# Kernel tuning notes

Hardware: AMD Instinct MI355X
Metric: run time of the kernel (lower is better)

## Reference

```python
import jax, jax.numpy as jnp
import numpy as np

M, TS, NX, NY = 24, 60, 192, 192   # solutions, source timesteps, source grid
H, D = 4, 8                         # num_heads, d_head
SIGMA = 0.2
N_TIME_STEPS = 50
T_MAX = 200.0
LX = 100.0                          # solutions[0]['params']['Lx']
SRC_T_MAX = 200.0                   # solutions[0]['params']['t_max']
NG = 50                             # target grid resolution (hard-coded in source)


def setup_inputs():
    key = jax.random.key(0)
    ks = jax.random.split(key, 8)
    c1_preds = jax.random.normal(ks[0], (M, TS, NX, NY), jnp.float32)
    c2_preds = jax.random.normal(ks[1], (M, TS, NX, NY), jnp.float32)
    lys = 30.0 + 90.0 * jax.random.uniform(ks[2], (M,), jnp.float32)
    c_cus = 0.0029 * jax.random.uniform(ks[3], (M,), jnp.float32)
    c_nis = 0.0018 * jax.random.uniform(ks[4], (M,), jnp.float32)
    params = jnp.stack([lys, c_cus, c_nis], axis=1)  # [M,3]
    # nonuniform, sorted per-solution y grid spanning [0, Ly_m]
    base = jnp.linspace(0.0, 1.0, NY, dtype=jnp.float32) ** 1.2
    src_y = lys[:, None] * base[None, :]  # [M,NY]
    src_t_last = 100.0 + 200.0 * jax.random.uniform(ks[5], (M,), jnp.float32)
    Wq = 0.3 * jax.random.normal(ks[6], (3, H * D), jnp.float32)
    Wk = 0.3 * jax.random.normal(ks[7], (3, H * D), jnp.float32)
    bq = jnp.zeros((H * D,), jnp.float32)
    bk = jnp.zeros((H * D,), jnp.float32)
    return dict(c1_preds=c1_preds, c2_preds=c2_preds, params=params, src_y=src_y,
                src_t_last=src_t_last, Wq=Wq, bq=bq, Wk=Wk, bk=bk,
                ly_target=jnp.float32(75.0), c_cu_target=jnp.float32(0.0015),
                c_ni_target=jnp.float32(0.0009))


def _axis_interp(grid, q):
    """1-D linear interp setup. grid [G] sorted, q [P] -> (idx, frac, in_bounds)."""
    G = grid.shape[-1]
    idx = jnp.clip(jnp.searchsorted(grid, q, side='right') - 1, 0, G - 2)
    g0 = jnp.take(grid, idx)
    g1 = jnp.take(grid, idx + 1)
    frac = (q - g0) / (g1 - g0)
    inb = (q >= grid[0]) & (q <= grid[-1])  # scipy fill_value=0 outside
    return idx, frac, inb


def reference(c1_preds, c2_preds, params, src_y, src_t_last, Wq, bq, Wk, bk,
              ly_target, c_cu_target, c_ni_target):
    lys, c_cus, c_nis = params[:, 0], params[:, 1], params[:, 2]
    # normalization exactly as in the torch forward
    ly_n = (lys - 30.0) / (120.0 - 30.0)
    cu_n = c_cus / 0.0029
    ni_n = c_nis / 0.0018
    t_ly = (ly_target - 30.0) / (120.0 - 30.0)
    t_cu = c_cu_target / 0.0029
    t_ni = c_ni_target / 0.0018

    p = jnp.stack([ly_n, cu_n, ni_n], axis=1)            # [M,3]
    tgt = jnp.stack([t_ly, t_cu, t_ni])[None, :]          # [1,3]
    Q = (tgt @ Wq + bq).reshape(H, D)                     # [H,D]
    K = (p @ Wk + bk).reshape(-1, H, D)                   # [M,H,D]
    logits = jnp.einsum('mhd,hd->mh', K, Q) / jnp.sqrt(jnp.float32(D))
    attn = jax.nn.softmax(logits, axis=0).mean(axis=1)    # softmax over solutions, mean heads -> [M]

    dist2 = ((ly_n - t_ly) ** 2 + (cu_n - t_cu) ** 2 + (ni_n - t_ni) ** 2) / SIGMA ** 2
    sw = jnp.exp(-dist2 / 2.0)
    sw = sw / (sw.sum() + 1e-12)
    w = attn * sw
    w = w / (w.sum() + 1e-12)
    w = jax.lax.stop_gradient(w)  # original detaches weights before interpolation

    # ---- physics-aware interpolation ----
    times = jnp.linspace(0.0, min(SRC_T_MAX, T_MAX), N_TIME_STEPS)  # [T]
    ti = jnp.clip(jnp.round(times[:, None] / src_t_last[None, :] * (TS - 1)).astype(jnp.int32),
                  0, TS - 1)                                         # [T,M]

    src_x = jnp.linspace(0.0, LX, NX)
    qx = jnp.linspace(0.0, LX, NG)
    qy = (jnp.arange(NG, dtype=jnp.float32) / (NG - 1)) * ly_target  # linspace(0, ly_target, NG)

    ix, fx, mx = _axis_interp(src_x, qx)                             # [NG] each (shared x grid)
    scale = ly_target / lys                                           # [M]
    y_scaled = src_y * scale[:, None]                                 # [M,NY]
    iy, fy, my = jax.vmap(lambda g: _axis_interp(g, qy))(y_scaled)    # [M,NG] each
    mask = (mx[None, :, None] & my[:, None, :]).astype(c1_preds.dtype)  # [M,NG,NG]

    T = N_TIME_STEPS
    iy_b = jnp.broadcast_to(iy[None, :, None, :], (T, M, NG, NG))
    iy1_b = jnp.broadcast_to((iy + 1)[None, :, None, :], (T, M, NG, NG))

    def interp_field(preds):
        vals = preds[jnp.arange(M)[None, :], ti]                      # [T,M,NX,NY] time gather
        fxc = fx[None, None, :, None]
        vx = vals[:, :, ix, :] * (1.0 - fxc) + vals[:, :, ix + 1, :] * fxc  # [T,M,NG,NY]
        v0 = jnp.take_along_axis(vx, iy_b, axis=3)                    # [T,M,NG,NG]
        v1 = jnp.take_along_axis(vx, iy1_b, axis=3)
        fyc = fy[None, :, None, :]
        v = (v0 * (1.0 - fyc) + v1 * fyc) * mask[None]
        return jnp.einsum('tmij,m->tij', v, w)                        # weighted sum over solutions

    c1 = interp_field(c1_preds).at[:, :, 0].set(c_cu_target)
    c2 = interp_field(c2_preds).at[:, :, -1].set(c_ni_target)
    return jnp.stack([c1, c2])  # [2, T, NG, NG]
```

## Files before the change

kernel.cpp:

```cpp
#include <hip/hip_runtime.h>
#include <math.h>

#define M   24
#define TS  60
#define NX  192
#define NY  192
#define H_  4
#define D_  8
#define NTS 50
#define NG  50

__device__ float g_w[M];
__device__ int   g_ti[NTS][M];
__device__ int   g_ix[NG];
__device__ float g_fx[NG];
__device__ float g_mx[NG];
__device__ int   g_iy[M][NG];
__device__ float g_fy[M][NG];
__device__ float g_my[M][NG];

__global__ __launch_bounds__(256) void prep_kernel(
    const float* __restrict__ params, const float* __restrict__ src_y,
    const float* __restrict__ stl,
    const float* __restrict__ Wq, const float* __restrict__ bq,
    const float* __restrict__ Wk, const float* __restrict__ bk,
    const float* __restrict__ lyt_p, const float* __restrict__ ccu_p,
    const float* __restrict__ cni_p)
{
    const int tid = threadIdx.x;
    __shared__ float s_logits[M][H_];
    __shared__ float s_sw[M];

    const float ly_target = lyt_p[0];
    const float c_cu_t = ccu_p[0];
    const float c_ni_t = cni_p[0];

    const float t_ly = (ly_target - 30.0f) / 90.0f;
    const float t_cu = c_cu_t / 0.0029f;
    const float t_ni = c_ni_t / 0.0018f;

    if (tid < M) {
        const int m = tid;
        const float ly  = params[m*3 + 0];
        const float ccu = params[m*3 + 1];
        const float cni = params[m*3 + 2];
        const float ly_n = (ly - 30.0f) / 90.0f;
        const float cu_n = ccu / 0.0029f;
        const float ni_n = cni / 0.0018f;
        for (int h = 0; h < H_; ++h) {
            float acc = 0.0f;
            for (int d = 0; d < D_; ++d) {
                const int col = h*D_ + d;
                const float q = t_ly*Wq[0*32+col] + t_cu*Wq[1*32+col] + t_ni*Wq[2*32+col] + bq[col];
                const float k = ly_n*Wk[0*32+col] + cu_n*Wk[1*32+col] + ni_n*Wk[2*32+col] + bk[col];
                acc += k * q;
            }
            s_logits[m][h] = acc / sqrtf(8.0f);
        }
        const float dly = ly_n - t_ly, dcu = cu_n - t_cu, dni = ni_n - t_ni;
        const float d2 = (dly*dly + dcu*dcu + dni*dni) / 0.04f;
        s_sw[m] = expf(-d2 * 0.5f);
    }
    __syncthreads();

    if (tid == 0) {
        float attn[M];
        for (int m = 0; m < M; ++m) attn[m] = 0.0f;
        for (int h = 0; h < H_; ++h) {
            float mxv = -1e30f;
            for (int m = 0; m < M; ++m) mxv = fmaxf(mxv, s_logits[m][h]);
            float e[M]; float s = 0.0f;
            for (int m = 0; m < M; ++m) { e[m] = expf(s_logits[m][h] - mxv); s += e[m]; }
            for (int m = 0; m < M; ++m) attn[m] += e[m] / s;
        }
        float ssw = 0.0f;
        for (int m = 0; m < M; ++m) ssw += s_sw[m];
        float w[M]; float wsum = 0.0f;
        for (int m = 0; m < M; ++m) {
            w[m] = (attn[m] * 0.25f) * (s_sw[m] / (ssw + 1e-12f));
            wsum += w[m];
        }
        for (int m = 0; m < M; ++m) g_w[m] = w[m] / (wsum + 1e-12f);
    }

    const float step_t = 200.0f / 49.0f;
    for (int idx = tid; idx < NTS*M; idx += blockDim.x) {
        const int t = idx / M, m = idx % M;
        const float tt = (t == NTS-1) ? 200.0f : step_t * (float)t;
        const float r = tt / stl[m] * 59.0f;
        int ti = (int)rintf(r);
        ti = ti < 0 ? 0 : (ti > TS-1 ? TS-1 : ti);
        g_ti[t][m] = ti;
    }

    if (tid < NG) {
        const int i = tid;
        const float step_x = 100.0f / 191.0f;
        const float step_q = 100.0f / 49.0f;
        const float q = (i == NG-1) ? 100.0f : step_q * (float)i;
        int pos = 0;
        for (int g = 0; g < NX; ++g) {
            const float gv = (g == NX-1) ? 100.0f : step_x * (float)g;
            if (gv <= q) pos = g + 1;
        }
        int id = pos - 1;
        id = id < 0 ? 0 : (id > NX-2 ? NX-2 : id);
        const float g0 = (id   == NX-1) ? 100.0f : step_x * (float)id;
        const float g1 = (id+1 == NX-1) ? 100.0f : step_x * (float)(id+1);
        g_ix[i] = id;
        g_fx[i] = (q - g0) / (g1 - g0);
        g_mx[i] = (q >= 0.0f && q <= 100.0f) ? 1.0f : 0.0f;
    }

    for (int idx = tid; idx < M*NG; idx += blockDim.x) {
        const int m = idx / NG, j = idx % NG;
        const float scale = ly_target / params[m*3 + 0];
        const float q = (float)j / 49.0f * ly_target;
        const float* sy = src_y + m*NY;
        int pos = 0;
        for (int g = 0; g < NY; ++g) {
            const float gv = sy[g] * scale;
            if (gv <= q) pos = g + 1;
        }
        int id = pos - 1;
        id = id < 0 ? 0 : (id > NY-2 ? NY-2 : id);
        const float g0 = sy[id] * scale;
        const float g1 = sy[id+1] * scale;
        g_iy[m][j] = id;
        g_fy[m][j] = (q - g0) / (g1 - g0);
        const float gfirst = sy[0] * scale;
        const float glast  = sy[NY-1] * scale;
        g_my[m][j] = (q >= gfirst && q <= glast) ? 1.0f : 0.0f;
    }
}

__global__ __launch_bounds__(256) void stage_kernel(
    const float* __restrict__ c1, const float* __restrict__ c2,
    float* __restrict__ partial)
{
    const int m = blockIdx.x;
    const int t = blockIdx.y;
    const int f = blockIdx.z;
    const int tid = threadIdx.x;

    __shared__ float xrow[NG][NY + 4];

    const float* __restrict__ preds = (f == 0) ? c1 : c2;
    const int tim = g_ti[t][m];
    const float* __restrict__ slice = preds + (((size_t)m * TS + tim) * NX) * (size_t)NY;

    for (int idx = tid; idx < NG * (NY / 4); idx += 256) {
        const int i  = idx / (NY / 4);
        const int y4 = (idx - i * (NY / 4)) * 4;
        const int   ixi = g_ix[i];
        const float fxi = g_fx[i];
        const float4 r0 = *(const float4*)(slice + (size_t)ixi * NY + y4);
        const float4 r1 = *(const float4*)(slice + (size_t)(ixi + 1) * NY + y4);
        float4 v;
        v.x = r0.x * (1.0f - fxi) + r1.x * fxi;
        v.y = r0.y * (1.0f - fxi) + r1.y * fxi;
        v.z = r0.z * (1.0f - fxi) + r1.z * fxi;
        v.w = r0.w * (1.0f - fxi) + r1.w * fxi;
        *(float4*)&xrow[i][y4] = v;
    }
    __syncthreads();

    const float wm = g_w[m];
    float* __restrict__ dst = partial + (((size_t)f * NTS + t) * M + m) * (size_t)(NG * NG);
    for (int idx = tid; idx < NG * NG; idx += 256) {
        const int i = idx / NG;
        const int j = idx - i * NG;
        const int   iyj = g_iy[m][j];
        const float fyj = g_fy[m][j];
        const float msk = g_mx[i] * g_my[m][j];
        const float v0 = xrow[i][iyj];
        const float v1 = xrow[i][iyj + 1];
        const float v = (v0 * (1.0f - fyj) + v1 * fyj) * msk;
        dst[idx] = v * wm;
    }
}

__global__ __launch_bounds__(256) void reduce_kernel(
    const float* __restrict__ partial, float* __restrict__ out,
    const float* __restrict__ ccu_p, const float* __restrict__ cni_p)
{
    const int idx = blockIdx.x * 256 + threadIdx.x;
    const int total = 2 * NTS * NG * NG;
    if (idx >= total) return;
    const int p  = idx % (NG * NG);
    const int ft = idx / (NG * NG);
    const int f  = ft / NTS;
    const int j  = p % NG;

    const float* __restrict__ src = partial + (size_t)ft * M * (NG * NG) + p;
    float acc = 0.0f;
    #pragma unroll
    for (int m = 0; m < M; ++m) acc += src[(size_t)m * (NG * NG)];

    if (f == 0 && j == 0)      acc = ccu_p[0];
    if (f == 1 && j == NG - 1) acc = cni_p[0];
    out[idx] = acc;
}

extern "C" void kernel_launch(void* const* d_in, const int* in_sizes, int n_in,
                              void* d_out, int out_size, void* d_ws, size_t ws_size,
                              hipStream_t stream) {
    const float* c1     = (const float*)d_in[0];
    const float* c2     = (const float*)d_in[1];
    const float* params = (const float*)d_in[2];
    const float* src_y  = (const float*)d_in[3];
    const float* stl    = (const float*)d_in[4];
    const float* Wq     = (const float*)d_in[5];
    const float* bq     = (const float*)d_in[6];
    const float* Wk     = (const float*)d_in[7];
    const float* bk     = (const float*)d_in[8];
    const float* lyt    = (const float*)d_in[9];
    const float* ccut   = (const float*)d_in[10];
    const float* cnit   = (const float*)d_in[11];
    float* out     = (float*)d_out;
    float* partial = (float*)d_ws;

    prep_kernel<<<1, 256, 0, stream>>>(params, src_y, stl, Wq, bq, Wk, bk, lyt, ccut, cnit);

    dim3 gridA(M, NTS, 2);
    stage_kernel<<<gridA, 256, 0, stream>>>(c1, c2, partial);

    const int total = 2 * NTS * NG * NG;
    reduce_kernel<<<(total + 255) / 256, 256, 0, stream>>>(partial, out, ccut, cnit);
}
```

Before: 432.0 us.

## Split stage blocks over row tiles, binary-search y grid, vectorize reduce

The stage kernel grid is doubled by splitting the 50 target rows into two 25-row tiles per block, which halves shared memory per block and raises parallelism and occupancy. The prep kernel's linear scan over the source y grid becomes a binary search, shortening the single-block serial prep. The reduce kernel now processes four outputs per thread with float4 loads and stores. The row split adds redundant per-block setup, and the float4 reduce relies on the 2500-element partial stride staying 16-byte aligned.

```diff
diff --git a/kernel.cpp b/kernel.cpp
--- a/kernel.cpp
+++ b/kernel.cpp
@@ -9,6 +9,7 @@
 #define D_  8
 #define NTS 50
 #define NG  50
+#define ITILE 25
 
 __device__ float g_w[M];
 __device__ int   g_ti[NTS][M];
@@ -117,12 +118,13 @@
         const float scale = ly_target / params[m*3 + 0];
         const float q = (float)j / 49.0f * ly_target;
         const float* sy = src_y + m*NY;
-        int pos = 0;
-        for (int g = 0; g < NY; ++g) {
-            const float gv = sy[g] * scale;
-            if (gv <= q) pos = g + 1;
-        }
-        int id = pos - 1;
+        int lo = 0, hi = NY;
+        while (lo < hi) {
+            const int mid = (lo + hi) >> 1;
+            const float gv = sy[mid] * scale;
+            if (gv <= q) lo = mid + 1; else hi = mid;
+        }
+        int id = lo - 1;
         id = id < 0 ? 0 : (id > NY-2 ? NY-2 : id);
         const float g0 = sy[id] * scale;
         const float g1 = sy[id+1] * scale;
@@ -138,20 +140,23 @@
     const float* __restrict__ c1, const float* __restrict__ c2,
     float* __restrict__ partial)
 {
-    const int m = blockIdx.x;
-    const int t = blockIdx.y;
-    const int f = blockIdx.z;
-    const int tid = threadIdx.x;
-
-    __shared__ float xrow[NG][NY + 4];
+    const int m    = blockIdx.x;
+    const int t    = blockIdx.y;
+    const int fz   = blockIdx.z;
+    const int f    = fz >> 1;
+    const int i0   = (fz & 1) * ITILE;
+    const int tid  = threadIdx.x;
+
+    __shared__ float xrow[ITILE][NY + 4];
 
     const float* __restrict__ preds = (f == 0) ? c1 : c2;
     const int tim = g_ti[t][m];
     const float* __restrict__ slice = preds + (((size_t)m * TS + tim) * NX) * (size_t)NY;
 
-    for (int idx = tid; idx < NG * (NY / 4); idx += 256) {
-        const int i  = idx / (NY / 4);
-        const int y4 = (idx - i * (NY / 4)) * 4;
+    for (int idx = tid; idx < ITILE * (NY / 4); idx += 256) {
+        const int il = idx / (NY / 4);
+        const int y4 = (idx - il * (NY / 4)) * 4;
+        const int i  = i0 + il;
         const int   ixi = g_ix[i];
         const float fxi = g_fx[i];
         const float4 r0 = *(const float4*)(slice + (size_t)ixi * NY + y4);
@@ -161,22 +166,23 @@
         v.y = r0.y * (1.0f - fxi) + r1.y * fxi;
         v.z = r0.z * (1.0f - fxi) + r1.z * fxi;
         v.w = r0.w * (1.0f - fxi) + r1.w * fxi;
-        *(float4*)&xrow[i][y4] = v;
+        *(float4*)&xrow[il][y4] = v;
     }
     __syncthreads();
 
     const float wm = g_w[m];
     float* __restrict__ dst = partial + (((size_t)f * NTS + t) * M + m) * (size_t)(NG * NG);
-    for (int idx = tid; idx < NG * NG; idx += 256) {
-        const int i = idx / NG;
-        const int j = idx - i * NG;
+    for (int idx = tid; idx < ITILE * NG; idx += 256) {
+        const int il = idx / NG;
+        const int j  = idx - il * NG;
+        const int i  = i0 + il;
         const int   iyj = g_iy[m][j];
         const float fyj = g_fy[m][j];
         const float msk = g_mx[i] * g_my[m][j];
-        const float v0 = xrow[i][iyj];
-        const float v1 = xrow[i][iyj + 1];
+        const float v0 = xrow[il][iyj];
+        const float v1 = xrow[il][iyj + 1];
         const float v = (v0 * (1.0f - fyj) + v1 * fyj) * msk;
-        dst[idx] = v * wm;
+        dst[i * NG + j] = v * wm;
     }
 }
 
@@ -184,22 +190,30 @@
     const float* __restrict__ partial, float* __restrict__ out,
     const float* __restrict__ ccu_p, const float* __restrict__ cni_p)
 {
-    const int idx = blockIdx.x * 256 + threadIdx.x;
-    const int total = 2 * NTS * NG * NG;
-    if (idx >= total) return;
-    const int p  = idx % (NG * NG);
-    const int ft = idx / (NG * NG);
-    const int f  = ft / NTS;
-    const int j  = p % NG;
+    const int q = blockIdx.x * 256 + threadIdx.x;
+    const int total4 = (2 * NTS * NG * NG) / 4;
+    if (q >= total4) return;
+    const int idx = q * 4;
+    const int p   = idx % (NG * NG);
+    const int ft  = idx / (NG * NG);
+    const int f   = ft / NTS;
 
     const float* __restrict__ src = partial + (size_t)ft * M * (NG * NG) + p;
-    float acc = 0.0f;
+    float4 acc = make_float4(0.f, 0.f, 0.f, 0.f);
     #pragma unroll
-    for (int m = 0; m < M; ++m) acc += src[(size_t)m * (NG * NG)];
-
-    if (f == 0 && j == 0)      acc = ccu_p[0];
-    if (f == 1 && j == NG - 1) acc = cni_p[0];
-    out[idx] = acc;
+    for (int m = 0; m < M; ++m) {
+        const float4 v = *(const float4*)(src + (size_t)m * (NG * NG));
+        acc.x += v.x; acc.y += v.y; acc.z += v.z; acc.w += v.w;
+    }
+
+    float vals[4] = {acc.x, acc.y, acc.z, acc.w};
+    #pragma unroll
+    for (int k = 0; k < 4; ++k) {
+        const int j = (p + k) % NG;
+        if (f == 0 && j == 0)      vals[k] = ccu_p[0];
+        if (f == 1 && j == NG - 1) vals[k] = cni_p[0];
+    }
+    *(float4*)(out + idx) = make_float4(vals[0], vals[1], vals[2], vals[3]);
 }
 
 extern "C" void kernel_launch(void* const* d_in, const int* in_sizes, int n_in,
@@ -222,9 +236,9 @@
 
     prep_kernel<<<1, 256, 0, stream>>>(params, src_y, stl, Wq, bq, Wk, bk, lyt, ccut, cnit);
 
-    dim3 gridA(M, NTS, 2);
+    dim3 gridA(M, NTS, 2 * (NG / ITILE));
     stage_kernel<<<gridA, 256, 0, stream>>>(c1, c2, partial);
 
-    const int total = 2 * NTS * NG * NG;
-    reduce_kernel<<<(total + 255) / 256, 256, 0, stream>>>(partial, out, ccut, cnit);
-}
+    const int total4 = (2 * NTS * NG * NG) / 4;
+    reduce_kernel<<<(total4 + 255) / 256, 256, 0, stream>>>(partial, out, ccut, cnit);
+}
```

Result: faster. 417.2 us (-3.4%).
